# Performance work log

Measured on AMD Instinct MI355X. Metric: run time of the kernel, lower is better.

Reference implementation:

```python
import jax, jax.numpy as jnp
import numpy as np

B, T, C = 4, 2048, 768
H, D = 12, 64          # num heads, head size
MLP = 3072
EPS = 1e-6
SCALE = C ** (-0.5)    # NOTE: source scales by n_embd**-0.5, not head_size**-0.5


def setup_inputs() -> dict:
    key = jax.random.key(0)
    ks = jax.random.split(key, 12)
    s = 0.02
    return {
        "x":     jax.random.normal(ks[0], (B, T, C), jnp.float32),
        "Wq":    jax.random.normal(ks[1], (H, C, D), jnp.float32) * s,
        "Wk":    jax.random.normal(ks[2], (H, C, D), jnp.float32) * s,
        "Wv":    jax.random.normal(ks[3], (H, C, D), jnp.float32) * s,
        "Wo":    jax.random.normal(ks[4], (H * D, C), jnp.float32) * s,
        "bo":    jnp.zeros((C,), jnp.float32),
        "ln1_g": jnp.ones((C,), jnp.float32),
        "ln1_b": jnp.zeros((C,), jnp.float32),
        "ln2_g": jnp.ones((C,), jnp.float32),
        "ln2_b": jnp.zeros((C,), jnp.float32),
        "W1":    jax.random.normal(ks[5], (C, MLP), jnp.float32) * s,
        "b1":    jnp.zeros((MLP,), jnp.float32),
        "W2":    jax.random.normal(ks[6], (MLP, C), jnp.float32) * s,
        "b2":    jnp.zeros((C,), jnp.float32),
    }


def _ln(x, g, b):
    mu = jnp.mean(x, axis=-1, keepdims=True)
    var = jnp.var(x, axis=-1, keepdims=True)
    return (x - mu) * jax.lax.rsqrt(var + EPS) * g + b


def reference(x, Wq, Wk, Wv, Wo, bo, ln1_g, ln1_b, ln2_g, ln2_b, W1, b1, W2, b2):
    xn = _ln(x, ln1_g, ln1_b)
    # batched per-head projections: [B,T,C] x [H,C,D] -> [B,H,T,D]
    q = jnp.einsum("btc,hcd->bhtd", xn, Wq)
    k = jnp.einsum("btc,hcd->bhtd", xn, Wk)
    v = jnp.einsum("btc,hcd->bhtd", xn, Wv)
    wei = jnp.einsum("bhtd,bhsd->bhts", q, k) * SCALE  # [B,H,T,T]
    wei = jax.nn.softmax(wei, axis=-1)
    attn = jnp.einsum("bhts,bhsd->bhtd", wei, v)
    # concat heads along feature dim (head order preserved)
    attn = attn.transpose(0, 2, 1, 3).reshape(B, T, H * D)
    sa = attn @ Wo + bo
    x2 = sa + x                      # residual 1 (dropout = identity in eval)
    y = _ln(x2, ln2_g, ln2_b)
    y = jax.nn.gelu(y @ W1 + b1, approximate=False) @ W2 + b2
    return x2 + y                    # residual 2
```

## Files before the change

### kernel.cpp

```cpp
#include <hip/hip_runtime.h>
#include <hip/hip_bf16.h>
#include <cstdint>
#include <cmath>

#define B_ 4
#define T_ 2048
#define C_ 768
#define H_ 12
#define D_ 64
#define MLP_ 3072
#define BT_ (B_*T_)

typedef __hip_bfloat16 hbf;
typedef __bf16 bf16_t;
typedef bf16_t bf16x8 __attribute__((ext_vector_type(8)));
typedef bf16_t bf16x4 __attribute__((ext_vector_type(4)));
typedef float f32x4 __attribute__((ext_vector_type(4)));

static __device__ __forceinline__ void load_lds16(const void* g, void* l) {
    __builtin_amdgcn_global_load_lds(
        (const __attribute__((address_space(1))) unsigned int*)g,
        (__attribute__((address_space(3))) unsigned int*)l, 16, 0, 0);
}

__global__ __launch_bounds__(256) void transpose_pack(
    const float* __restrict__ src, hbf* __restrict__ dst, int R, int S)
{
    __shared__ float tl[64 * 65];
    src += (size_t)blockIdx.z * R * S;
    dst += (size_t)blockIdx.z * R * S;
    const int r0 = blockIdx.y * 64, s0 = blockIdx.x * 64;
    const int c = threadIdx.x & 63, q = threadIdx.x >> 6;
#pragma unroll
    for (int j = 0; j < 16; ++j) {
        int r = q + j * 4;
        tl[r * 65 + c] = src[(size_t)(r0 + r) * S + s0 + c];
    }
    __syncthreads();
#pragma unroll
    for (int j = 0; j < 16; ++j) {
        int s = q + j * 4;
        dst[(size_t)(s0 + s) * R + r0 + c] = __float2bfloat16(tl[c * 65 + s]);
    }
}

__global__ __launch_bounds__(256) void pack_qkv3(
    const float* __restrict__ Wq, const float* __restrict__ Wk,
    const float* __restrict__ Wv, hbf* __restrict__ WqkT)
{
    __shared__ float tl[64 * 65];
    const int z = blockIdx.z;
    const int mtx = z / 12, head = z - mtx * 12;
    const float* src = (mtx == 0 ? Wq : mtx == 1 ? Wk : Wv) + (size_t)head * 49152;
    hbf* dst = WqkT + (size_t)z * 49152;
    const int r0 = blockIdx.y * 64;
    const int c = threadIdx.x & 63, q = threadIdx.x >> 6;
#pragma unroll
    for (int j = 0; j < 16; ++j) {
        int r = q + j * 4;
        tl[r * 65 + c] = src[(size_t)(r0 + r) * 64 + c];
    }
    __syncthreads();
#pragma unroll
    for (int j = 0; j < 16; ++j) {
        int s = q + j * 4;
        dst[(size_t)s * 768 + r0 + c] = __float2bfloat16(tl[c * 65 + s]);
    }
}

template<typename TI>
__global__ __launch_bounds__(256) void ln_kernel(
    const TI* __restrict__ x, const float* __restrict__ g,
    const float* __restrict__ bb, hbf* __restrict__ out)
{
    __shared__ float red[8];
    const int row = blockIdx.x;
    const TI* xr = x + (size_t)row * C_;
    const int t = threadIdx.x;
    float v0, v1, v2;
    if constexpr (__is_same(TI, float)) {
        v0 = xr[t]; v1 = xr[t + 256]; v2 = xr[t + 512];
    } else {
        v0 = __bfloat162float(xr[t]);
        v1 = __bfloat162float(xr[t + 256]);
        v2 = __bfloat162float(xr[t + 512]);
    }
    float s = v0 + v1 + v2;
    float s2 = v0 * v0 + v1 * v1 + v2 * v2;
#pragma unroll
    for (int m = 1; m < 64; m <<= 1) {
        s  += __shfl_xor(s,  m, 64);
        s2 += __shfl_xor(s2, m, 64);
    }
    if ((t & 63) == 0) { red[t >> 6] = s; red[4 + (t >> 6)] = s2; }
    __syncthreads();
    float S  = red[0] + red[1] + red[2] + red[3];
    float S2 = red[4] + red[5] + red[6] + red[7];
    float mu  = S * (1.0f / C_);
    float var = S2 * (1.0f / C_) - mu * mu;
    float inv = rsqrtf(var + 1e-6f);
    hbf* orow = out + (size_t)row * C_;
    orow[t]       = __float2bfloat16((v0 - mu) * inv * g[t]       + bb[t]);
    orow[t + 256] = __float2bfloat16((v1 - mu) * inv * g[t + 256] + bb[t + 256]);
    orow[t + 512] = __float2bfloat16((v2 - mu) * inv * g[t + 512] + bb[t + 512]);
}

template<int EPI, int TN>
__global__ __launch_bounds__(256, (TN == 64) ? 4 : 3) void gemm_kernel(
    const hbf* __restrict__ A, const hbf* __restrict__ Bt,
    float* __restrict__ outF, hbf* __restrict__ outH,
    const float* __restrict__ bias, const float* __restrict__ residF,
    const hbf* __restrict__ residH,
    int M, int N, int K,
    hbf* __restrict__ qb, hbf* __restrict__ kb, hbf* __restrict__ vt,
    float scale, int gx)
{
    constexpr int AM = (TN == 128) ? 4 : 2;
    constexpr int NB_B = (TN == 128) ? 4 : 2;
    __shared__ hbf sA[128 * 64];
    __shared__ hbf sB[TN * 64];
    const int tid = threadIdx.x;
    const int lane = tid & 63;
    const int wid = tid >> 6;
    const int lr = lane & 15, hg = lane >> 4;
    const int bid = blockIdx.x, nwg = gridDim.x;
    const int wg = (bid & 7) * (nwg >> 3) + (bid >> 3);
    const int bx = wg % gx, by = wg / gx;
    const int row0 = by * 128;
    const int col0 = bx * TN;
    const int wrow = (TN == 128) ? (wid >> 1) * 64 : wid * 32;
    const int wcol = (TN == 128) ? (wid & 1) * 64 : 0;

    f32x4 acc[AM][4] = {};

    int offG[4];
    const int Kb = K * 2;
#pragma unroll
    for (int i = 0; i < 4; ++i) {
        int c = tid + i * 256;
        offG[i] = (c >> 3) * Kb + (((c & 7) ^ ((c >> 3) & 7)) << 4);
    }
    const char* gA = (const char*)(A + (size_t)row0 * K);
    const char* gB = (const char*)(Bt + (size_t)col0 * K);

    auto stage = [&](int kt) {
        const int kb2 = kt * 128;
#pragma unroll
        for (int i = 0; i < 4; ++i)
            load_lds16(gA + (size_t)(offG[i] + kb2), (char*)sA + i * 4096 + wid * 1024);
#pragma unroll
        for (int i = 0; i < NB_B; ++i)
            load_lds16(gB + (size_t)(offG[i] + kb2), (char*)sB + i * 4096 + wid * 1024);
    };

    const int NK = K >> 6;
    stage(0);
    for (int kt = 0; kt < NK; ++kt) {
        __syncthreads();
#pragma unroll
        for (int kf = 0; kf < 2; ++kf) {
            const int sl = ((kf * 4 + hg) ^ (lr & 7)) << 4;
            bf16x8 af[AM], bfr[4];
#pragma unroll
            for (int m = 0; m < AM; ++m)
                af[m] = *(const bf16x8*)((const char*)sA + (wrow + m * 16 + lr) * 128 + sl);
#pragma unroll
            for (int n = 0; n < 4; ++n)
                bfr[n] = *(const bf16x8*)((const char*)sB + (wcol + n * 16 + lr) * 128 + sl);
#pragma unroll
            for (int m = 0; m < AM; ++m)
#pragma unroll
                for (int n = 0; n < 4; ++n)
                    acc[m][n] = __builtin_amdgcn_mfma_f32_16x16x32_bf16(af[m], bfr[n], acc[m][n], 0, 0, 0);
        }
        __syncthreads();
        if (kt + 1 < NK) stage(kt + 1);
    }

#pragma unroll
    for (int m = 0; m < AM; ++m) {
#pragma unroll
        for (int n = 0; n < 4; ++n) {
            const int colc = col0 + wcol + n * 16 + lr;
            const int rowb = row0 + wrow + m * 16 + hg * 4;
            if constexpr (EPI == 3) {
                if (colc >= 2 * C_) {
                    bf16x4 w;
#pragma unroll
                    for (int j = 0; j < 4; ++j) w[j] = (bf16_t)acc[m][n][j];
                    *(bf16x4*)(vt + (size_t)(colc - 2 * C_) * BT_ + rowb) = w;
                    continue;
                }
            }
#pragma unroll
            for (int j = 0; j < 4; ++j) {
                int row = rowb + j;
                int col = colc;
                float v = acc[m][n][j];
                if constexpr (EPI == 0) {
                    outH[(size_t)row * N + col] = __float2bfloat16(v);
                } else if constexpr (EPI == 2) {
                    float tt = v + bias[col];
                    float ge = 0.5f * tt * (1.0f + erff(tt * 0.70710678118654752f));
                    outH[(size_t)row * N + col] = __float2bfloat16(ge);
                } else if constexpr (EPI == 3) {
                    int typ = col / C_;
                    int rr = col - typ * C_;
                    int h = rr >> 6, d = rr & 63;
                    int b = row >> 11, t = row & (T_ - 1);
                    size_t bh = (size_t)b * H_ + h;
                    if (typ == 0) qb[(bh * T_ + t) * D_ + d] = __float2bfloat16(v * scale);
                    else          kb[(bh * T_ + t) * D_ + d] = __float2bfloat16(v);
                } else if constexpr (EPI == 4) {
                    outH[(size_t)row * N + col] =
                        __float2bfloat16(v + bias[col] + residF[(size_t)row * N + col]);
                } else {
                    outF[(size_t)row * N + col] =
                        v + bias[col] + __bfloat162float(residH[(size_t)row * N + col]);
                }
            }
        }
    }
}

__global__ __launch_bounds__(256, 3) void attn_kernel(
    const hbf* __restrict__ qg, const hbf* __restrict__ kg,
    const hbf* __restrict__ vg, hbf* __restrict__ outA)
{
    __shared__ hbf sK0[64 * 64], sK1[64 * 64];
    __shared__ hbf sV0[64 * 64], sV1[64 * 64];
    __shared__ hbf sP[4 * 32 * 64];
    const int tid = threadIdx.x, lane = tid & 63, wid = tid >> 6;
    const int lr = lane & 15, hg = lane >> 4;
    const int wg = (blockIdx.x & 7) * 96 + (blockIdx.x >> 3);
    const int bh = wg >> 4;
    const int b = bh / H_, h = bh - b * H_;
    const int wr0 = (wg & 15) * 128 + wid * 32;
    const hbf* qbh = qg + (size_t)bh * T_ * D_;
    const hbf* kbh = kg + (size_t)bh * T_ * D_;
    const hbf* vbh = vg + (size_t)h * 64 * BT_ + (size_t)b * T_;

    bf16x8 a_q[2][2];
#pragma unroll
    for (int m = 0; m < 2; ++m)
#pragma unroll
        for (int kf = 0; kf < 2; ++kf)
            a_q[m][kf] = *(const bf16x8*)(qbh + (size_t)(wr0 + m * 16 + lr) * D_ + kf * 32 + hg * 8);

    bf16x8 vone;
#pragma unroll
    for (int i = 0; i < 8; ++i) vone[i] = (bf16_t)1.0f;

    f32x4 o[2][4] = {};
    f32x4 lden[2] = {};
    float mreg[2] = {-3e38f, -3e38f};

    int offK[2], offV[2];
#pragma unroll
    for (int i = 0; i < 2; ++i) {
        int c = tid + i * 256;
        int sw = ((c & 7) ^ ((c >> 3) & 7)) << 4;
        offK[i] = (c >> 3) * 128 + sw;
        offV[i] = (c >> 3) * (BT_ * 2) + sw;
    }
    hbf* sPw = sP + wid * (32 * 64);
    const int sl0 = ((0 * 4 + hg) ^ (lr & 7)) << 4;
    const int sl1 = ((1 * 4 + hg) ^ (lr & 7)) << 4;
    const int bcast = hg * 20;

    auto stage = [&](int itn, hbf* sKd, hbf* sVd) {
        const char* kp = (const char*)kbh + (size_t)itn * 8192;
        const char* vp = (const char*)vbh + (size_t)itn * 128;
#pragma unroll
        for (int i = 0; i < 2; ++i) {
            load_lds16(kp + offK[i], (char*)sKd + i * 4096 + wid * 1024);
            load_lds16(vp + offV[i], (char*)sVd + i * 4096 + wid * 1024);
        }
    };

    auto tile = [&](const hbf* sKc, const hbf* sVc) {
        f32x4 st[4][2] = {};
        __builtin_amdgcn_s_setprio(1);
#pragma unroll
        for (int kf = 0; kf < 2; ++kf) {
            const int sl = kf ? sl1 : sl0;
#pragma unroll
            for (int n = 0; n < 4; ++n) {
                bf16x8 ak = *(const bf16x8*)((const char*)sKc + (n * 16 + lr) * 128 + sl);
                st[n][0] = __builtin_amdgcn_mfma_f32_16x16x32_bf16(ak, a_q[0][kf], st[n][0], 0, 0, 0);
                st[n][1] = __builtin_amdgcn_mfma_f32_16x16x32_bf16(ak, a_q[1][kf], st[n][1], 0, 0, 0);
            }
        }
        __builtin_amdgcn_s_setprio(0);

#pragma unroll
        for (int m = 0; m < 2; ++m) {
            float t01, t23, a0, a1;
            f32x4 mx = st[0][m];
            mx[0] = fmaxf(mx[0], st[1][m][0]); mx[1] = fmaxf(mx[1], st[1][m][1]);
            mx[2] = fmaxf(mx[2], st[1][m][2]); mx[3] = fmaxf(mx[3], st[1][m][3]);
            f32x4 my = st[2][m];
            my[0] = fmaxf(my[0], st[3][m][0]); my[1] = fmaxf(my[1], st[3][m][1]);
            my[2] = fmaxf(my[2], st[3][m][2]); my[3] = fmaxf(my[3], st[3][m][3]);
            t01 = fmaxf(fmaxf(mx[0], my[0]), fmaxf(mx[1], my[1]));
            t23 = fmaxf(fmaxf(mx[2], my[2]), fmaxf(mx[3], my[3]));
            float t = fmaxf(t01, t23);
            t = fmaxf(t, __shfl_xor(t, 16, 64));
            t = fmaxf(t, __shfl_xor(t, 32, 64));
            if (__any(t - mreg[m] > 8.0f)) {
                float nm = fmaxf(mreg[m], t);
                float fac = __expf(mreg[m] - nm);
                mreg[m] = nm;
                float fb[4];
#pragma unroll
                for (int j = 0; j < 4; ++j)
                    fb[j] = __shfl(fac, bcast + j, 64);
#pragma unroll
                for (int j = 0; j < 4; ++j) {
                    lden[m][j] *= fb[j];
#pragma unroll
                    for (int nd = 0; nd < 4; ++nd)
                        o[m][nd][j] *= fb[j];
                }
            }
            const int r = m * 16 + lr;
#pragma unroll
            for (int n = 0; n < 4; ++n) {
                float p0 = __expf(st[n][m][0] - mreg[m]);
                float p1 = __expf(st[n][m][1] - mreg[m]);
                float p2 = __expf(st[n][m][2] - mreg[m]);
                float p3 = __expf(st[n][m][3] - mreg[m]);
                bf16x4 w;
                w[0] = (bf16_t)p0; w[1] = (bf16_t)p1; w[2] = (bf16_t)p2; w[3] = (bf16_t)p3;
                *(bf16x4*)((char*)sPw + r * 128 +
                           (((n * 2 + (hg >> 1)) ^ (r & 7)) << 4) + ((hg & 1) * 8)) = w;
            }
        }

        __builtin_amdgcn_s_setprio(1);
#pragma unroll
        for (int kf = 0; kf < 2; ++kf) {
            const int sl = kf ? sl1 : sl0;
            bf16x8 ap0 = *(const bf16x8*)((const char*)sPw + lr * 128 + sl);
            bf16x8 ap1 = *(const bf16x8*)((const char*)sPw + (16 + lr) * 128 + sl);
            lden[0] = __builtin_amdgcn_mfma_f32_16x16x32_bf16(ap0, vone, lden[0], 0, 0, 0);
            lden[1] = __builtin_amdgcn_mfma_f32_16x16x32_bf16(ap1, vone, lden[1], 0, 0, 0);
#pragma unroll
            for (int nd = 0; nd < 4; ++nd) {
                bf16x8 bv = *(const bf16x8*)((const char*)sVc + (nd * 16 + lr) * 128 + sl);
                o[0][nd] = __builtin_amdgcn_mfma_f32_16x16x32_bf16(ap0, bv, o[0][nd], 0, 0, 0);
                o[1][nd] = __builtin_amdgcn_mfma_f32_16x16x32_bf16(ap1, bv, o[1][nd], 0, 0, 0);
            }
        }
        __builtin_amdgcn_s_setprio(0);
    };

    const int NT = T_ / 64;
    stage(0, sK0, sV0);
    __syncthreads();
    for (int it = 0; it < NT; it += 2) {
        stage(it + 1, sK1, sV1);
        tile(sK0, sV0);
        __syncthreads();
        if (it + 2 < NT) stage(it + 2, sK0, sV0);
        tile(sK1, sV1);
        __syncthreads();
    }

#pragma unroll
    for (int m = 0; m < 2; ++m) {
        f32x4 rinv;
#pragma unroll
        for (int j = 0; j < 4; ++j) rinv[j] = 1.0f / lden[m][j];
#pragma unroll
        for (int nd = 0; nd < 4; ++nd)
#pragma unroll
            for (int j = 0; j < 4; ++j) {
                int row = wr0 + m * 16 + hg * 4 + j;
                int col = nd * 16 + lr;
                outA[((size_t)(b * T_ + row)) * C_ + h * D_ + col] =
                    __float2bfloat16(o[m][nd][j] * rinv[j]);
            }
    }
}

extern "C" void kernel_launch(void* const* d_in, const int* in_sizes, int n_in,
                              void* d_out, int out_size, void* d_ws, size_t ws_size,
                              hipStream_t stream)
{
    const float* x    = (const float*)d_in[0];
    const float* Wq   = (const float*)d_in[1];
    const float* Wk   = (const float*)d_in[2];
    const float* Wv   = (const float*)d_in[3];
    const float* Wo   = (const float*)d_in[4];
    const float* bo   = (const float*)d_in[5];
    const float* ln1g = (const float*)d_in[6];
    const float* ln1b = (const float*)d_in[7];
    const float* ln2g = (const float*)d_in[8];
    const float* ln2b = (const float*)d_in[9];
    const float* W1   = (const float*)d_in[10];
    const float* b1   = (const float*)d_in[11];
    const float* W2   = (const float*)d_in[12];
    const float* b2   = (const float*)d_in[13];
    float* out = (float*)d_out;
    char* ws = (char*)d_ws;

    hbf*  xn    = (hbf*)(ws + 0);
    hbf*  WqkT  = (hbf*)(ws + 12582912);
    hbf*  qb    = (hbf*)(ws + 16121856);
    hbf*  kb    = (hbf*)(ws + 28704768);
    hbf*  vT    = (hbf*)(ws + 41287680);
    hbf*  h1    = (hbf*)(ws + 0);
    hbf*  attnB = (hbf*)(ws + 53870592);
    hbf*  yln   = (hbf*)(ws + 53870592);
    hbf*  x2b   = (hbf*)(ws + 66453504);
    hbf*  WoT   = (hbf*)(ws + 91619328);
    hbf*  W1T   = (hbf*)(ws + 92798976);
    hbf*  W2T   = (hbf*)(ws + 97517568);

    const float SCALE = 0.036084391824351615f;

    pack_qkv3<<<dim3(1, 12, 36), 256, 0, stream>>>(Wq, Wk, Wv, WqkT);
    transpose_pack<<<dim3(12, 12, 1), 256, 0, stream>>>(Wo, WoT, 768, 768);
    transpose_pack<<<dim3(48, 12, 1), 256, 0, stream>>>(W1, W1T, 768, 3072);
    transpose_pack<<<dim3(12, 48, 1), 256, 0, stream>>>(W2, W2T, 3072, 768);
    ln_kernel<float><<<8192, 256, 0, stream>>>(x, ln1g, ln1b, xn);
    gemm_kernel<3,128><<<1152, 256, 0, stream>>>(xn, WqkT, nullptr, nullptr, nullptr, nullptr,
        nullptr, 8192, 2304, 768, qb, kb, vT, SCALE, 18);
    attn_kernel<<<768, 256, 0, stream>>>(qb, kb, vT, attnB);
    gemm_kernel<4,64><<<768, 256, 0, stream>>>(attnB, WoT, nullptr, x2b, bo, x,
        nullptr, 8192, 768, 768, nullptr, nullptr, nullptr, 1.0f, 12);
    ln_kernel<hbf><<<8192, 256, 0, stream>>>(x2b, ln2g, ln2b, yln);
    gemm_kernel<2,128><<<1536, 256, 0, stream>>>(yln, W1T, nullptr, h1, b1, nullptr,
        nullptr, 8192, 3072, 768, nullptr, nullptr, nullptr, 1.0f, 24);
    gemm_kernel<5,64><<<768, 256, 0, stream>>>(h1, W2T, out, nullptr, b2, nullptr,
        x2b, 8192, 768, 3072, nullptr, nullptr, nullptr, 1.0f, 12);
}
```

Measured before the change: 280.1 us.

## Double-buffer LDS in narrow GEMMs and switch attention softmax to exp2

The TN=64 GEMMs (output projection and MLP down-projection) now keep two LDS buffers, so the global-to-LDS load of the next K-tile overlaps MFMA work on the current one. Their occupancy hint drops from 4 to 3 waves to make room for the larger shared memory. Separately, the log2(e) factor is folded into the Q scaling so attention softmax can call the hardware exp2 directly instead of __expf. The lazy-rescale threshold is raised to match the base-2 domain. Both GEMM loops assume an even number of K-tiles, which holds for K=768 and K=3072.

```diff
diff --git a/kernel.cpp b/kernel.cpp
--- a/kernel.cpp
+++ b/kernel.cpp
@@ -106,7 +106,7 @@
 }
 
 template<int EPI, int TN>
-__global__ __launch_bounds__(256, (TN == 64) ? 4 : 3) void gemm_kernel(
+__global__ __launch_bounds__(256, (TN == 64) ? 3 : 3) void gemm_kernel(
     const hbf* __restrict__ A, const hbf* __restrict__ Bt,
     float* __restrict__ outF, hbf* __restrict__ outH,
     const float* __restrict__ bias, const float* __restrict__ residF,
@@ -115,10 +115,13 @@
     hbf* __restrict__ qb, hbf* __restrict__ kb, hbf* __restrict__ vt,
     float scale, int gx)
 {
+    constexpr bool DBUF = (TN == 64);
     constexpr int AM = (TN == 128) ? 4 : 2;
     constexpr int NB_B = (TN == 128) ? 4 : 2;
-    __shared__ hbf sA[128 * 64];
-    __shared__ hbf sB[TN * 64];
+    constexpr int ABYTES = 128 * 64 * 2;
+    constexpr int BBYTES = TN * 64 * 2;
+    __shared__ hbf sA[(DBUF ? 2 : 1) * 128 * 64];
+    __shared__ hbf sB[(DBUF ? 2 : 1) * TN * 64];
     const int tid = threadIdx.x;
     const int lane = tid & 63;
     const int wid = tid >> 6;
@@ -143,38 +146,58 @@
     const char* gA = (const char*)(A + (size_t)row0 * K);
     const char* gB = (const char*)(Bt + (size_t)col0 * K);
 
-    auto stage = [&](int kt) {
+    auto stage = [&](int kt, int which) {
         const int kb2 = kt * 128;
+        char* dA = (char*)sA + which * ABYTES;
+        char* dB = (char*)sB + which * BBYTES;
 #pragma unroll
         for (int i = 0; i < 4; ++i)
-            load_lds16(gA + (size_t)(offG[i] + kb2), (char*)sA + i * 4096 + wid * 1024);
+            load_lds16(gA + (size_t)(offG[i] + kb2), dA + i * 4096 + wid * 1024);
 #pragma unroll
         for (int i = 0; i < NB_B; ++i)
-            load_lds16(gB + (size_t)(offG[i] + kb2), (char*)sB + i * 4096 + wid * 1024);
+            load_lds16(gB + (size_t)(offG[i] + kb2), dB + i * 4096 + wid * 1024);
     };
-
-    const int NK = K >> 6;
-    stage(0);
-    for (int kt = 0; kt < NK; ++kt) {
-        __syncthreads();
+    auto compute = [&](int which) {
+        const char* cA = (const char*)sA + which * ABYTES;
+        const char* cB = (const char*)sB + which * BBYTES;
 #pragma unroll
         for (int kf = 0; kf < 2; ++kf) {
             const int sl = ((kf * 4 + hg) ^ (lr & 7)) << 4;
             bf16x8 af[AM], bfr[4];
 #pragma unroll
             for (int m = 0; m < AM; ++m)
-                af[m] = *(const bf16x8*)((const char*)sA + (wrow + m * 16 + lr) * 128 + sl);
+                af[m] = *(const bf16x8*)(cA + (wrow + m * 16 + lr) * 128 + sl);
 #pragma unroll
             for (int n = 0; n < 4; ++n)
-                bfr[n] = *(const bf16x8*)((const char*)sB + (wcol + n * 16 + lr) * 128 + sl);
+                bfr[n] = *(const bf16x8*)(cB + (wcol + n * 16 + lr) * 128 + sl);
 #pragma unroll
             for (int m = 0; m < AM; ++m)
 #pragma unroll
                 for (int n = 0; n < 4; ++n)
                     acc[m][n] = __builtin_amdgcn_mfma_f32_16x16x32_bf16(af[m], bfr[n], acc[m][n], 0, 0, 0);
         }
+    };
+
+    const int NK = K >> 6;
+    if constexpr (DBUF) {
+        stage(0, 0);
         __syncthreads();
-        if (kt + 1 < NK) stage(kt + 1);
+        for (int kt = 0; kt < NK; kt += 2) {
+            stage(kt + 1, 1);
+            compute(0);
+            __syncthreads();
+            if (kt + 2 < NK) stage(kt + 2, 0);
+            compute(1);
+            __syncthreads();
+        }
+    } else {
+        stage(0, 0);
+        for (int kt = 0; kt < NK; ++kt) {
+            __syncthreads();
+            compute(0);
+            __syncthreads();
+            if (kt + 1 < NK) stage(kt + 1, 0);
+        }
     }
 
 #pragma unroll
@@ -295,21 +318,20 @@
 
 #pragma unroll
         for (int m = 0; m < 2; ++m) {
-            float t01, t23, a0, a1;
             f32x4 mx = st[0][m];
             mx[0] = fmaxf(mx[0], st[1][m][0]); mx[1] = fmaxf(mx[1], st[1][m][1]);
             mx[2] = fmaxf(mx[2], st[1][m][2]); mx[3] = fmaxf(mx[3], st[1][m][3]);
             f32x4 my = st[2][m];
             my[0] = fmaxf(my[0], st[3][m][0]); my[1] = fmaxf(my[1], st[3][m][1]);
             my[2] = fmaxf(my[2], st[3][m][2]); my[3] = fmaxf(my[3], st[3][m][3]);
-            t01 = fmaxf(fmaxf(mx[0], my[0]), fmaxf(mx[1], my[1]));
-            t23 = fmaxf(fmaxf(mx[2], my[2]), fmaxf(mx[3], my[3]));
+            float t01 = fmaxf(fmaxf(mx[0], my[0]), fmaxf(mx[1], my[1]));
+            float t23 = fmaxf(fmaxf(mx[2], my[2]), fmaxf(mx[3], my[3]));
             float t = fmaxf(t01, t23);
             t = fmaxf(t, __shfl_xor(t, 16, 64));
             t = fmaxf(t, __shfl_xor(t, 32, 64));
-            if (__any(t - mreg[m] > 8.0f)) {
+            if (__any(t - mreg[m] > 11.5415603f)) {
                 float nm = fmaxf(mreg[m], t);
-                float fac = __expf(mreg[m] - nm);
+                float fac = __builtin_amdgcn_exp2f(mreg[m] - nm);
                 mreg[m] = nm;
                 float fb[4];
 #pragma unroll
@@ -326,10 +348,10 @@
             const int r = m * 16 + lr;
 #pragma unroll
             for (int n = 0; n < 4; ++n) {
-                float p0 = __expf(st[n][m][0] - mreg[m]);
-                float p1 = __expf(st[n][m][1] - mreg[m]);
-                float p2 = __expf(st[n][m][2] - mreg[m]);
-                float p3 = __expf(st[n][m][3] - mreg[m]);
+                float p0 = __builtin_amdgcn_exp2f(st[n][m][0] - mreg[m]);
+                float p1 = __builtin_amdgcn_exp2f(st[n][m][1] - mreg[m]);
+                float p2 = __builtin_amdgcn_exp2f(st[n][m][2] - mreg[m]);
+                float p3 = __builtin_amdgcn_exp2f(st[n][m][3] - mreg[m]);
                 bf16x4 w;
                 w[0] = (bf16_t)p0; w[1] = (bf16_t)p1; w[2] = (bf16_t)p2; w[3] = (bf16_t)p3;
                 *(bf16x4*)((char*)sPw + r * 128 +
@@ -418,7 +440,7 @@
     hbf*  W1T   = (hbf*)(ws + 92798976);
     hbf*  W2T   = (hbf*)(ws + 97517568);
 
-    const float SCALE = 0.036084391824351615f;
+    const float SCALE2 = 0.036084391824351615f * 1.4426950408889634f;
 
     pack_qkv3<<<dim3(1, 12, 36), 256, 0, stream>>>(Wq, Wk, Wv, WqkT);
     transpose_pack<<<dim3(12, 12, 1), 256, 0, stream>>>(Wo, WoT, 768, 768);
@@ -426,7 +448,7 @@
     transpose_pack<<<dim3(12, 48, 1), 256, 0, stream>>>(W2, W2T, 3072, 768);
     ln_kernel<float><<<8192, 256, 0, stream>>>(x, ln1g, ln1b, xn);
     gemm_kernel<3,128><<<1152, 256, 0, stream>>>(xn, WqkT, nullptr, nullptr, nullptr, nullptr,
-        nullptr, 8192, 2304, 768, qb, kb, vT, SCALE, 18);
+        nullptr, 8192, 2304, 768, qb, kb, vT, SCALE2, 18);
     attn_kernel<<<768, 256, 0, stream>>>(qb, kb, vT, attnB);
     gemm_kernel<4,64><<<768, 256, 0, stream>>>(attnB, WoT, nullptr, x2b, bo, x,
         nullptr, 8192, 768, 768, nullptr, nullptr, nullptr, 1.0f, 12);
```

Result: slower. 287.6 us (+2.7%).
